# Kernel tuning notes

Measured on AMD Instinct MI355X. Metric: run time of the kernel, lower is better.

Reference implementation:

```python
import jax, jax.numpy as jnp
import numpy as np

B, C, F = 1024, 63, 250
H, D = 4, 250          # heads, out_channels per head
TOP_K = 8
NEG_SLOPE = 0.2


def setup_inputs() -> dict:
    key = jax.random.key(0)
    ks = jax.random.split(key, 7)
    x = jax.random.normal(ks[0], (B, 1, C, F), dtype=jnp.float32)
    W_gat = jax.random.normal(ks[1], (F, H * D), dtype=jnp.float32) / jnp.sqrt(jnp.float32(F))
    att_src = jax.random.normal(ks[2], (H, D), dtype=jnp.float32) * 0.1
    att_dst = jax.random.normal(ks[3], (H, D), dtype=jnp.float32) * 0.1
    bias_gat = jax.random.normal(ks[4], (H * D,), dtype=jnp.float32) * 0.02
    W_proj = jax.random.normal(ks[5], (H * D, D), dtype=jnp.float32) / jnp.sqrt(jnp.float32(H * D))
    b_proj = jax.random.normal(ks[6], (D,), dtype=jnp.float32) * 0.02
    return {"x": x, "W_gat": W_gat, "att_src": att_src, "att_dst": att_dst,
            "bias_gat": bias_gat, "W_proj": W_proj, "b_proj": b_proj}


def reference(x, W_gat, att_src, att_dst, bias_gat, W_proj, b_proj):
    # ---- correlation adjacency over the batch (non-differentiable mask path) ----
    xa = x[:, 0]                                             # [B, C, F]
    xc = xa - xa.mean(axis=-1, keepdims=True)
    xn = xc / (jnp.std(xc, axis=-1, ddof=1, keepdims=True) + 1e-8)  # unbiased std like torch
    adj = jnp.einsum('bcf,bdf->bcd', xn, xn) / jnp.float32(F)       # bmm / Fdim
    adj = adj.mean(axis=0)                                   # [C, C]
    topv, _ = jax.lax.top_k(adj, TOP_K)                      # per-row top-k
    thresh = topv[:, -1:]                                    # [C, 1]
    mask = (adj >= thresh) & (adj != 0)                      # nonzeros kept by dense_to_sparse
    eye = jnp.eye(C, dtype=bool)
    # GATConv: remove_self_loops then add_self_loops -> exactly one self loop per node
    mask_full = (mask & ~eye) | eye                          # [i(src), j(dst)]

    # ---- GATConv (edge_attr ignored: edge_dim=None -> lin_edge is None) ----
    h = (x.reshape(B * C, F) @ W_gat).reshape(B, C, H, D)    # [B, C, H, D]
    # edges only connect nodes 0..C-1 of the flattened (B*C) node tensor = batch 0
    h0 = h[0]                                                # [C, H, D]
    a_s = jnp.einsum('chd,hd->ch', h0, att_src)              # source logits
    a_d = jnp.einsum('chd,hd->ch', h0, att_dst)              # destination logits
    e = jax.nn.leaky_relu(a_s[:, None, :] + a_d[None, :, :], NEG_SLOPE)  # [i, j, h]
    logits = jnp.where(mask_full[:, :, None], e, -jnp.inf)
    w = jax.nn.softmax(logits, axis=0)                       # normalize over sources i per target j
    att0 = jnp.einsum('ijh,ihd->jhd', w, h0)                 # [C, H, D]
    # nodes >= C have only a self loop -> softmax weight 1 -> output = h
    y = h.at[0].set(att0)
    y = y.reshape(B * C, H * D) + bias_gat

    out = y @ W_proj + b_proj                                # [B*C, D]
    return out.reshape(B, C, -1)[:, None]                    # [B, 1, C, D]
```

## Files before the change

kernel.cpp:

```cpp
#include <hip/hip_runtime.h>
#include <math.h>

#define NB 1024
#define NC 63
#define NF 250
#define NH 4
#define ND 250
#define NHD 1000

typedef __bf16 bf16x8 __attribute__((ext_vector_type(8)));
typedef float f32x4 __attribute__((ext_vector_type(4)));

__global__ __launch_bounds__(256) void k_fused(const float* __restrict__ x,
                                               const __bf16* __restrict__ WcT,
                                               const float* __restrict__ biasc,
                                               float* __restrict__ out,
                                               float* __restrict__ partial) {
    __shared__ __align__(16) __bf16 Xh[64 * 256];
    __shared__ __align__(16) __bf16 Xl[64 * 256];
    float* const momS = (float*)Xh;
    const int t = threadIdx.x;
    const int w = t >> 6, l = t & 63;
    const int l16 = l & 15, lq = l >> 4;
    const int swz = (l16 & 7) << 3;
    const int nb = w * 64;

    {
        const int kz = t ^ 56;
        Xh[63 * 256 + kz] = (__bf16)1.0f;
        Xl[63 * 256 + kz] = (__bf16)0.0f;
    }

    float bc[4];
#pragma unroll
    for (int ni = 0; ni < 4; ++ni) {
        const int col = nb + ni * 16 + l16;
        bc[ni] = (col < ND) ? biasc[col] : 0.f;
    }

    const f32x4 z4 = {0.f, 0.f, 0.f, 0.f};
    const int b = blockIdx.x;
    const float* xb = x + (size_t)b * (NC * NF);

#pragma unroll
    for (int it = 0; it < 8; ++it) {
        const int u = it * 256 + t;
        if (u < 2016) {
            const int row = u >> 5;
            const int ko = (u & 31) << 3;
            const float* src = xb + row * NF + ko;
            float v[8];
#pragma unroll
            for (int q = 0; q < 4; ++q) {
                if (ko + q * 2 < NF) {
                    const float2 p = *(const float2*)(src + q * 2);
                    v[2 * q] = p.x; v[2 * q + 1] = p.y;
                } else { v[2 * q] = 0.f; v[2 * q + 1] = 0.f; }
            }
            bf16x8 h, lo_;
#pragma unroll
            for (int j = 0; j < 8; ++j) {
                h[j] = (__bf16)v[j];
                lo_[j] = (__bf16)(v[j] - (float)h[j]);
            }
            const int kS = ko ^ ((row & 7) << 3);
            *(bf16x8*)&Xh[row * 256 + kS] = h;
            *(bf16x8*)&Xl[row * 256 + kS] = lo_;
        }
    }
    __syncthreads();

    bf16x8 bfr[4][4];
    f32x4 accM[4][4];
    f32x4 accG[4];
#pragma unroll
    for (int mi = 0; mi < 4; ++mi)
#pragma unroll
        for (int ni = 0; ni < 4; ++ni) accM[mi][ni] = z4;
#pragma unroll
    for (int ni = 0; ni < 4; ++ni) accG[ni] = z4;

    const int garow = (16 * w + l16) * 256;

#pragma unroll
    for (int ni = 0; ni < 4; ++ni) {
        const int n = nb + ni * 16 + l16;
#pragma unroll
        for (int kk = 0; kk < 4; ++kk)
            bfr[ni][kk] = *(const bf16x8*)(WcT + (size_t)n * 256 + kk * 32 + lq * 8);
    }
#pragma unroll
    for (int kk = 0; kk < 4; ++kk) {
        const int kb = (kk * 32 + lq * 8) ^ swz;
        bf16x8 hi[4], lo[4];
#pragma unroll
        for (int r = 0; r < 4; ++r) {
            hi[r] = *(const bf16x8*)&Xh[(r * 16 + l16) * 256 + kb];
            lo[r] = *(const bf16x8*)&Xl[(r * 16 + l16) * 256 + kb];
        }
        const bf16x8 ah = *(const bf16x8*)&Xh[garow + kb];
        const bf16x8 al = *(const bf16x8*)&Xl[garow + kb];
#pragma unroll
        for (int mi = 0; mi < 4; ++mi)
#pragma unroll
            for (int ni = 0; ni < 4; ++ni)
                accM[mi][ni] = __builtin_amdgcn_mfma_f32_16x16x32_bf16(
                    hi[mi], bfr[ni][kk], accM[mi][ni], 0, 0, 0);
#pragma unroll
        for (int ni = 0; ni < 4; ++ni) {
            accG[ni] = __builtin_amdgcn_mfma_f32_16x16x32_bf16(ah, hi[ni], accG[ni], 0, 0, 0);
            accG[ni] = __builtin_amdgcn_mfma_f32_16x16x32_bf16(ah, lo[ni], accG[ni], 0, 0, 0);
            accG[ni] = __builtin_amdgcn_mfma_f32_16x16x32_bf16(al, hi[ni], accG[ni], 0, 0, 0);
        }
    }

#pragma unroll
    for (int ni = 0; ni < 4; ++ni) {
        const int n = nb + ni * 16 + l16;
#pragma unroll
        for (int kk = 0; kk < 4; ++kk)
            bfr[ni][kk] = *(const bf16x8*)(WcT + (size_t)n * 256 + (4 + kk) * 32 + lq * 8);
    }
#pragma unroll
    for (int kk = 0; kk < 4; ++kk) {
        const int kb = ((4 + kk) * 32 + lq * 8) ^ swz;
        bf16x8 hi[4], lo[4];
#pragma unroll
        for (int r = 0; r < 4; ++r) {
            hi[r] = *(const bf16x8*)&Xh[(r * 16 + l16) * 256 + kb];
            lo[r] = *(const bf16x8*)&Xl[(r * 16 + l16) * 256 + kb];
        }
        const bf16x8 ah = *(const bf16x8*)&Xh[garow + kb];
        const bf16x8 al = *(const bf16x8*)&Xl[garow + kb];
#pragma unroll
        for (int mi = 0; mi < 4; ++mi)
#pragma unroll
            for (int ni = 0; ni < 4; ++ni)
                accM[mi][ni] = __builtin_amdgcn_mfma_f32_16x16x32_bf16(
                    hi[mi], bfr[ni][kk], accM[mi][ni], 0, 0, 0);
#pragma unroll
        for (int ni = 0; ni < 4; ++ni) {
            accG[ni] = __builtin_amdgcn_mfma_f32_16x16x32_bf16(ah, hi[ni], accG[ni], 0, 0, 0);
            accG[ni] = __builtin_amdgcn_mfma_f32_16x16x32_bf16(ah, lo[ni], accG[ni], 0, 0, 0);
            accG[ni] = __builtin_amdgcn_mfma_f32_16x16x32_bf16(al, hi[ni], accG[ni], 0, 0, 0);
        }
    }

    __syncthreads();

    if (l16 == 15) {
#pragma unroll
        for (int r = 0; r < 4; ++r) momS[16 * w + lq * 4 + r] = accG[3][r];
    }
    if ((l16 >> 2) == lq) momS[64 + 16 * w + l16] = accG[w][l16 & 3];
    __syncthreads();
    if (t < 64) {
        const float S = momS[t], SSv = momS[64 + t];
        float m = S * (1.f / (float)NF);
        const float var = (SSv - S * S * (1.f / (float)NF)) * (1.f / (float)(NF - 1));
        float sc = 1.f / (sqrtf(var) + 1e-8f);
        if (t >= NC) { m = 0.f; sc = 0.f; }
        momS[128 + t] = m; momS[192 + t] = sc;
    }
    __syncthreads();

    float mr[4], sr[4];
#pragma unroll
    for (int r = 0; r < 4; ++r) {
        const int row = 16 * w + lq * 4 + r;
        mr[r] = momS[128 + row]; sr[r] = momS[192 + row];
    }
#pragma unroll
    for (int ni = 0; ni < 4; ++ni) {
        const float mc = momS[128 + 16 * ni + l16];
        const float sc = momS[192 + 16 * ni + l16];
#pragma unroll
        for (int r = 0; r < 4; ++r) {
            const int row = 16 * w + lq * 4 + r;
            const int col = 16 * ni + l16;
            partial[(size_t)b * 4096 + row * 64 + col] =
                (accG[ni][r] - (float)NF * mr[r] * mc) * sr[r] * sc;
        }
    }

    const size_t ob = (size_t)b * NC;
#pragma unroll
    for (int mi = 0; mi < 4; ++mi) {
#pragma unroll
        for (int r = 0; r < 4; ++r) {
            const int rt = mi * 16 + lq * 4 + r;
            if (rt < NC) {
#pragma unroll
                for (int ni = 0; ni < 4; ++ni) {
                    const int col = nb + ni * 16 + l16;
                    if (col < ND)
                        out[(ob + rt) * ND + col] = accM[mi][ni][r] + bc[ni];
                }
            }
        }
    }
}

__global__ __launch_bounds__(512) void k_adj_reduce(const float* __restrict__ partial,
                                                    float* __restrict__ adj) {
    __shared__ float red[8][64];
    const int row = blockIdx.x, t = threadIdx.x;
    const int c = t & 63, g = t >> 6;
    float s = 0.f;
    const float* p = partial + (size_t)(g * 128) * 4096 + row * 64 + c;
#pragma unroll 8
    for (int i = 0; i < 128; ++i) s += p[(size_t)i * 4096];
    red[g][c] = s;
    __syncthreads();
    if (t < NC) {
        float tot = 0.f;
#pragma unroll
        for (int gg = 0; gg < 8; ++gg) tot += red[gg][t];
        adj[row * NC + t] = tot * (1.f / ((float)NF * (float)NB));
    }
}

__global__ __launch_bounds__(256) void k_gs(const float* __restrict__ Wg,
                                            const float* __restrict__ att_src,
                                            const float* __restrict__ att_dst,
                                            float* __restrict__ gs,
                                            float* __restrict__ gd) {
    const int f = blockIdx.x;
    const int h = threadIdx.x >> 6, l = threadIdx.x & 63;
    const float* wr = Wg + (size_t)f * NHD + h * ND;
    const float* sp = att_src + h * ND;
    const float* dp = att_dst + h * ND;
    float s = 0.f, d = 0.f;
#pragma unroll
    for (int q = 0; q < 4; ++q) {
        const int dd = l + q * 64;
        if (dd < ND) {
            const float wv = wr[dd];
            s += wv * sp[dd];
            d += wv * dp[dd];
        }
    }
#pragma unroll
    for (int off = 32; off >= 1; off >>= 1) {
        s += __shfl_down(s, off);
        d += __shfl_down(d, off);
    }
    if (l == 0) { gs[f * NH + h] = s; gd[f * NH + h] = d; }
}

__global__ __launch_bounds__(512) void k_asad(const float* __restrict__ x,
                                              const float* __restrict__ gs,
                                              const float* __restrict__ gd,
                                              float* __restrict__ as_,
                                              float* __restrict__ ad_) {
    __shared__ float x0S[NC * NF];
    __shared__ float gsS[NF * NH], gdS[NF * NH];
    const int t = threadIdx.x;
    for (int e = t; e < NC * NF; e += 512) x0S[e] = x[e];
    for (int e = t; e < NF * NH; e += 512) { gsS[e] = gs[e]; gdS[e] = gd[e]; }
    __syncthreads();
    if (t < NC * NH) {
        const int c = t >> 2, h = t & 3;
        float s = 0.f, d = 0.f;
#pragma unroll 5
        for (int f = 0; f < NF; ++f) {
            const float xv = x0S[c * NF + f];
            s += xv * gsS[f * NH + h];
            d += xv * gdS[f * NH + h];
        }
        as_[t] = s; ad_[t] = d;
    }
}

__global__ __launch_bounds__(512) void k_out0(const float* __restrict__ adj,
                                              const float* __restrict__ as_,
                                              const float* __restrict__ ad_,
                                              const float* __restrict__ hp,
                                              const float* __restrict__ biasc,
                                              float* __restrict__ out) {
    __shared__ float adjS[NC * NC];
    __shared__ float thS[NC];
    __shared__ float asS[NC * 5];
    __shared__ float adS[NC * NH];
    __shared__ float wS[256];
    __shared__ float psum[2][256];
    const int j = blockIdx.x, t = threadIdx.x;
    const int w = t >> 6, l = t & 63;

    for (int e = t; e < NC * NC; e += 512) adjS[e] = adj[e];
    if (t < NC * NH) { asS[(t >> 2) * 5 + (t & 3)] = as_[t]; adS[t] = ad_[t]; }
    __syncthreads();

    for (int r = w; r < NC; r += 8) {
        const float v = (l < NC) ? adjS[r * NC + l] : -INFINITY;
        float prev = INFINITY;
        int krem = 8;
        float th = -INFINITY;
#pragma unroll
        for (int iter = 0; iter < 8; ++iter) {
            const float vm = (v < prev) ? v : -INFINITY;
            float m = vm;
#pragma unroll
            for (int off = 32; off >= 1; off >>= 1) m = fmaxf(m, __shfl_xor(m, off));
            const unsigned long long b = __ballot(vm == m);
            const int cnt = __popcll(b);
            if (cnt >= krem) { th = m; break; }
            krem -= cnt; prev = m;
        }
        if (l == 0) thS[r] = th;
    }
    __syncthreads();

    if (w < NH) {
        const int h = w, i = l;
        const float adv = adS[j * NH + h];
        const float a = (i < NC) ? adjS[i * NC + j] : 0.f;
        const bool msk = (i < NC) && ((i == j) || ((a >= thS[i]) && (a != 0.f)));
        float e = 0.f;
        if (msk) { e = asS[i * 5 + h] + adv; e = e > 0.f ? e : 0.2f * e; }
        float m = msk ? e : -INFINITY;
#pragma unroll
        for (int off = 32; off >= 1; off >>= 1) m = fmaxf(m, __shfl_xor(m, off));
        const float p = msk ? __expf(e - m) : 0.f;
        float s = p;
#pragma unroll
        for (int off = 32; off >= 1; off >>= 1) s += __shfl_xor(s, off);
        wS[(h << 6) + l] = p / s;
    }
    __syncthreads();

    const int q = t >> 8, col = t & 255;
    float acc = 0.f;
    const float* hpc = hp + col;
#pragma unroll 8
    for (int e = q * 128; e < q * 128 + 128; ++e)
        acc += wS[e] * hpc[(size_t)e * 256];
    psum[q][col] = acc;
    __syncthreads();
    if (t < ND) out[(size_t)j * ND + t] = psum[0][t] + psum[1][t] + biasc[t];
}

__global__ __launch_bounds__(256) void k_wc_part(const float* __restrict__ Wg,
                                                 const float* __restrict__ bias_gat,
                                                 const float* __restrict__ Wp,
                                                 float* __restrict__ pWcT,
                                                 float* __restrict__ pbias) {
    __shared__ float rows[250];
    const int b = blockIdx.x, t = threadIdx.x;
    if (b < 1000) {
        const int fb = (b >> 3) * 2, kq = b & 7;
        if (t < 250)
            rows[t] = Wg[(size_t)(fb + t / 125) * NHD + kq * 125 + (t % 125)];
        __syncthreads();
        if (t < ND) {
            float a0 = 0.f, a1 = 0.f;
            const float* wp = Wp + (size_t)(kq * 125) * ND + t;
            for (int k = 0; k < 125; ++k) {
                float wv = wp[(size_t)k * ND];
                a0 += rows[k] * wv;
                a1 += rows[125 + k] * wv;
            }
            pWcT[(size_t)kq * 65536 + (size_t)t * 256 + fb] = a0;
            pWcT[(size_t)kq * 65536 + (size_t)t * 256 + fb + 1] = a1;
        }
    } else {
        const int kq = b - 1000;
        if (t < ND) {
            float acc = 0.f;
            for (int k = kq * 125; k < kq * 125 + 125; ++k)
                acc += bias_gat[k] * Wp[(size_t)k * ND + t];
            pbias[kq * 256 + t] = acc;
        }
    }
}

__global__ __launch_bounds__(256) void k_wct(const float* __restrict__ pWcT,
                                             const float* __restrict__ pbias,
                                             const float* __restrict__ b_proj,
                                             __bf16* __restrict__ WcT,
                                             __bf16* __restrict__ WchT,
                                             float* __restrict__ biasc) {
    const int n = blockIdx.x, t = threadIdx.x;
    if (n < 256) {
        float v[8];
        float tot = 0.f;
#pragma unroll
        for (int kq = 0; kq < 8; ++kq) {
            float xv = 0.f;
            if (n < ND && t < NF) xv = pWcT[(size_t)kq * 65536 + (size_t)n * 256 + t];
            v[kq] = xv; tot += xv;
        }
        WcT[n * 256 + t] = (__bf16)tot;
#pragma unroll
        for (int h = 0; h < NH; ++h)
            WchT[h * 65536 + n * 256 + t] = (__bf16)(v[2 * h] + v[2 * h + 1]);
    } else {
        if (t < ND) {
            float v = 0.f;
#pragma unroll
            for (int kq = 0; kq < 8; ++kq) v += pbias[kq * 256 + t];
            biasc[t] = v + b_proj[t];
        }
    }
}

__global__ __launch_bounds__(256) void k_hp(const float* __restrict__ x,
                                            const __bf16* __restrict__ WchT,
                                            float* __restrict__ hp) {
    __shared__ __align__(16) __bf16 Xs[64 * 256];
    const int h = blockIdx.x;
    const int t = threadIdx.x;
    const int w = t >> 6, l = t & 63;
    const int l16 = l & 15, lq = l >> 4;
    const int nb = w * 64;
    const int swz = (l16 & 7) << 3;

    bf16x8 bfr[4][8];
    const __bf16* Wh = WchT + h * 65536;
#pragma unroll
    for (int ni = 0; ni < 4; ++ni) {
        const int n = nb + ni * 16 + l16;
#pragma unroll
        for (int kc = 0; kc < 8; ++kc)
            bfr[ni][kc] = *(const bf16x8*)(Wh + (size_t)n * 256 + kc * 32 + lq * 8);
    }

#pragma unroll
    for (int it = 0; it < 8; ++it) {
        const int u = it * 256 + t;
        const int row = u >> 5;
        const int ko = (u & 31) << 3;
        float v[8];
#pragma unroll
        for (int q = 0; q < 4; ++q) { v[2 * q] = 0.f; v[2 * q + 1] = 0.f; }
        if (row < NC) {
            const float* src = x + row * NF + ko;
#pragma unroll
            for (int q = 0; q < 4; ++q) {
                if (ko + 2 * q + 1 < NF) {
                    const float2 p = *(const float2*)(src + 2 * q);
                    v[2 * q] = p.x; v[2 * q + 1] = p.y;
                }
            }
        }
        bf16x8 hv;
#pragma unroll
        for (int jj = 0; jj < 8; ++jj) hv[jj] = (__bf16)v[jj];
        *(bf16x8*)&Xs[row * 256 + (ko ^ ((row & 7) << 3))] = hv;
    }
    __syncthreads();

    f32x4 acc[4][4];
    const f32x4 z4 = {0.f, 0.f, 0.f, 0.f};
#pragma unroll
    for (int mi = 0; mi < 4; ++mi)
#pragma unroll
        for (int ni = 0; ni < 4; ++ni) acc[mi][ni] = z4;

#pragma unroll
    for (int kc = 0; kc < 8; ++kc) {
        const int kb = (kc * 32 + lq * 8) ^ swz;
        bf16x8 afr[4];
#pragma unroll
        for (int mi = 0; mi < 4; ++mi)
            afr[mi] = *(const bf16x8*)&Xs[(mi * 16 + l16) * 256 + kb];
#pragma unroll
        for (int mi = 0; mi < 4; ++mi)
#pragma unroll
            for (int ni = 0; ni < 4; ++ni)
                acc[mi][ni] = __builtin_amdgcn_mfma_f32_16x16x32_bf16(
                    afr[mi], bfr[ni][kc], acc[mi][ni], 0, 0, 0);
    }

#pragma unroll
    for (int mi = 0; mi < 4; ++mi)
#pragma unroll
        for (int r = 0; r < 4; ++r) {
            const int row = mi * 16 + lq * 4 + r;
#pragma unroll
            for (int ni = 0; ni < 4; ++ni) {
                const int col = nb + ni * 16 + l16;
                hp[(size_t)(h * 64 + row) * 256 + col] = acc[mi][ni][r];
            }
        }
}

extern "C" void kernel_launch(void* const* d_in, const int* in_sizes, int n_in,
                              void* d_out, int out_size, void* d_ws, size_t ws_size,
                              hipStream_t stream) {
    const float* x       = (const float*)d_in[0];
    const float* Wg      = (const float*)d_in[1];
    const float* att_src = (const float*)d_in[2];
    const float* att_dst = (const float*)d_in[3];
    const float* bias_g  = (const float*)d_in[4];
    const float* Wp      = (const float*)d_in[5];
    const float* b_proj  = (const float*)d_in[6];
    float* out = (float*)d_out;
    float* ws  = (float*)d_ws;

    __bf16* WcT    = (__bf16*)ws;
    __bf16* WchT   = (__bf16*)(ws + 32768);
    float* pWcT    = ws + 32768 + 131072;
    float* pbias   = pWcT + 8 * 65536;
    float* biasc   = pbias + 2048;
    float* partial = biasc + 256;
    float* adj     = partial + 1024 * 4096;
    float* hp      = adj + NC * NC;
    float* gs      = hp + 65536;
    float* gd      = gs + 1000;
    float* as_     = gd + 1000;
    float* ad_     = as_ + 252;

    k_wc_part<<<1008, 256, 0, stream>>>(Wg, bias_g, Wp, pWcT, pbias);
    k_wct<<<257, 256, 0, stream>>>(pWcT, pbias, b_proj, WcT, WchT, biasc);
    k_fused<<<1024, 256, 0, stream>>>(x, WcT, biasc, out, partial);
    k_adj_reduce<<<63, 512, 0, stream>>>(partial, adj);
    k_gs<<<250, 256, 0, stream>>>(Wg, att_src, att_dst, gs, gd);
    k_asad<<<1, 512, 0, stream>>>(x, gs, gd, as_, ad_);
    k_hp<<<4, 256, 0, stream>>>(x, WchT, hp);
    k_out0<<<63, 512, 0, stream>>>(adj, as_, ad_, hp, biasc, out);
}
```

Before: 122.4 us.

## Stage X in two K-halves to halve shared memory and raise occupancy

Shared tiles for the hi/lo bf16 split of x shrink from 256 to 128 columns. The K dimension is now loaded and consumed in two halves, with a barrier between them. The ones-row used for moment sums is rebuilt per half and masked past F. Launch bounds now request 4 blocks per CU. The aim is to fit more concurrent blocks so global loads of one block overlap MFMA work of others. In exchange there is an extra sync and serialized load/compute phases within each block, and register pressure may force spills under the tighter bound.

```diff
diff --git a/kernel.cpp b/kernel.cpp
--- a/kernel.cpp
+++ b/kernel.cpp
@@ -11,13 +11,13 @@
 typedef __bf16 bf16x8 __attribute__((ext_vector_type(8)));
 typedef float f32x4 __attribute__((ext_vector_type(4)));
 
-__global__ __launch_bounds__(256) void k_fused(const float* __restrict__ x,
-                                               const __bf16* __restrict__ WcT,
-                                               const float* __restrict__ biasc,
-                                               float* __restrict__ out,
-                                               float* __restrict__ partial) {
-    __shared__ __align__(16) __bf16 Xh[64 * 256];
-    __shared__ __align__(16) __bf16 Xl[64 * 256];
+__global__ __launch_bounds__(256, 4) void k_fused(const float* __restrict__ x,
+                                                  const __bf16* __restrict__ WcT,
+                                                  const float* __restrict__ biasc,
+                                                  float* __restrict__ out,
+                                                  float* __restrict__ partial) {
+    __shared__ __align__(16) __bf16 Xh[64 * 128];
+    __shared__ __align__(16) __bf16 Xl[64 * 128];
     float* const momS = (float*)Xh;
     const int t = threadIdx.x;
     const int w = t >> 6, l = t & 63;
@@ -25,12 +25,6 @@
     const int swz = (l16 & 7) << 3;
     const int nb = w * 64;
 
-    {
-        const int kz = t ^ 56;
-        Xh[63 * 256 + kz] = (__bf16)1.0f;
-        Xl[63 * 256 + kz] = (__bf16)0.0f;
-    }
-
     float bc[4];
 #pragma unroll
     for (int ni = 0; ni < 4; ++ni) {
@@ -41,34 +35,7 @@
     const f32x4 z4 = {0.f, 0.f, 0.f, 0.f};
     const int b = blockIdx.x;
     const float* xb = x + (size_t)b * (NC * NF);
-
-#pragma unroll
-    for (int it = 0; it < 8; ++it) {
-        const int u = it * 256 + t;
-        if (u < 2016) {
-            const int row = u >> 5;
-            const int ko = (u & 31) << 3;
-            const float* src = xb + row * NF + ko;
-            float v[8];
-#pragma unroll
-            for (int q = 0; q < 4; ++q) {
-                if (ko + q * 2 < NF) {
-                    const float2 p = *(const float2*)(src + q * 2);
-                    v[2 * q] = p.x; v[2 * q + 1] = p.y;
-                } else { v[2 * q] = 0.f; v[2 * q + 1] = 0.f; }
-            }
-            bf16x8 h, lo_;
-#pragma unroll
-            for (int j = 0; j < 8; ++j) {
-                h[j] = (__bf16)v[j];
-                lo_[j] = (__bf16)(v[j] - (float)h[j]);
-            }
-            const int kS = ko ^ ((row & 7) << 3);
-            *(bf16x8*)&Xh[row * 256 + kS] = h;
-            *(bf16x8*)&Xl[row * 256 + kS] = lo_;
-        }
-    }
-    __syncthreads();
+    const int garow = (16 * w + l16) * 128;
 
     bf16x8 bfr[4][4];
     f32x4 accM[4][4];
@@ -80,69 +47,75 @@
 #pragma unroll
     for (int ni = 0; ni < 4; ++ni) accG[ni] = z4;
 
-    const int garow = (16 * w + l16) * 256;
-
-#pragma unroll
-    for (int ni = 0; ni < 4; ++ni) {
-        const int n = nb + ni * 16 + l16;
-#pragma unroll
-        for (int kk = 0; kk < 4; ++kk)
-            bfr[ni][kk] = *(const bf16x8*)(WcT + (size_t)n * 256 + kk * 32 + lq * 8);
-    }
-#pragma unroll
-    for (int kk = 0; kk < 4; ++kk) {
-        const int kb = (kk * 32 + lq * 8) ^ swz;
-        bf16x8 hi[4], lo[4];
-#pragma unroll
-        for (int r = 0; r < 4; ++r) {
-            hi[r] = *(const bf16x8*)&Xh[(r * 16 + l16) * 256 + kb];
-            lo[r] = *(const bf16x8*)&Xl[(r * 16 + l16) * 256 + kb];
-        }
-        const bf16x8 ah = *(const bf16x8*)&Xh[garow + kb];
-        const bf16x8 al = *(const bf16x8*)&Xl[garow + kb];
-#pragma unroll
-        for (int mi = 0; mi < 4; ++mi)
-#pragma unroll
-            for (int ni = 0; ni < 4; ++ni)
-                accM[mi][ni] = __builtin_amdgcn_mfma_f32_16x16x32_bf16(
-                    hi[mi], bfr[ni][kk], accM[mi][ni], 0, 0, 0);
+#pragma unroll
+    for (int h = 0; h < 2; ++h) {
+        if (h) __syncthreads();
+
+#pragma unroll
+        for (int it = 0; it < 4; ++it) {
+            const int u = it * 256 + t;
+            if (u < 1008) {
+                const int row = u >> 4;
+                const int ko = (u & 15) << 3;
+                const int kg = h * 128 + ko;
+                const float* src = xb + row * NF + kg;
+                float v[8];
+#pragma unroll
+                for (int q = 0; q < 4; ++q) {
+                    if (kg + q * 2 + 1 < NF) {
+                        const float2 p = *(const float2*)(src + q * 2);
+                        v[2 * q] = p.x; v[2 * q + 1] = p.y;
+                    } else { v[2 * q] = 0.f; v[2 * q + 1] = 0.f; }
+                }
+                bf16x8 hv, lo_;
+#pragma unroll
+                for (int j = 0; j < 8; ++j) {
+                    hv[j] = (__bf16)v[j];
+                    lo_[j] = (__bf16)(v[j] - (float)hv[j]);
+                }
+                const int kS = ko ^ ((row & 7) << 3);
+                *(bf16x8*)&Xh[row * 128 + kS] = hv;
+                *(bf16x8*)&Xl[row * 128 + kS] = lo_;
+            }
+        }
+        if (t < 128) {
+            const int kz = t ^ 56;
+            Xh[63 * 128 + kz] = (h * 128 + t < NF) ? (__bf16)1.0f : (__bf16)0.0f;
+            Xl[63 * 128 + kz] = (__bf16)0.0f;
+        }
+        __syncthreads();
+
 #pragma unroll
         for (int ni = 0; ni < 4; ++ni) {
-            accG[ni] = __builtin_amdgcn_mfma_f32_16x16x32_bf16(ah, hi[ni], accG[ni], 0, 0, 0);
-            accG[ni] = __builtin_amdgcn_mfma_f32_16x16x32_bf16(ah, lo[ni], accG[ni], 0, 0, 0);
-            accG[ni] = __builtin_amdgcn_mfma_f32_16x16x32_bf16(al, hi[ni], accG[ni], 0, 0, 0);
-        }
-    }
-
-#pragma unroll
-    for (int ni = 0; ni < 4; ++ni) {
-        const int n = nb + ni * 16 + l16;
-#pragma unroll
-        for (int kk = 0; kk < 4; ++kk)
-            bfr[ni][kk] = *(const bf16x8*)(WcT + (size_t)n * 256 + (4 + kk) * 32 + lq * 8);
-    }
-#pragma unroll
-    for (int kk = 0; kk < 4; ++kk) {
-        const int kb = ((4 + kk) * 32 + lq * 8) ^ swz;
-        bf16x8 hi[4], lo[4];
-#pragma unroll
-        for (int r = 0; r < 4; ++r) {
-            hi[r] = *(const bf16x8*)&Xh[(r * 16 + l16) * 256 + kb];
-            lo[r] = *(const bf16x8*)&Xl[(r * 16 + l16) * 256 + kb];
-        }
-        const bf16x8 ah = *(const bf16x8*)&Xh[garow + kb];
-        const bf16x8 al = *(const bf16x8*)&Xl[garow + kb];
-#pragma unroll
-        for (int mi = 0; mi < 4; ++mi)
-#pragma unroll
-            for (int ni = 0; ni < 4; ++ni)
-                accM[mi][ni] = __builtin_amdgcn_mfma_f32_16x16x32_bf16(
-                    hi[mi], bfr[ni][kk], accM[mi][ni], 0, 0, 0);
-#pragma unroll
-        for (int ni = 0; ni < 4; ++ni) {
-            accG[ni] = __builtin_amdgcn_mfma_f32_16x16x32_bf16(ah, hi[ni], accG[ni], 0, 0, 0);
-            accG[ni] = __builtin_amdgcn_mfma_f32_16x16x32_bf16(ah, lo[ni], accG[ni], 0, 0, 0);
-            accG[ni] = __builtin_amdgcn_mfma_f32_16x16x32_bf16(al, hi[ni], accG[ni], 0, 0, 0);
+            const int n = nb + ni * 16 + l16;
+#pragma unroll
+            for (int kk = 0; kk < 4; ++kk)
+                bfr[ni][kk] = *(const bf16x8*)(WcT + (size_t)n * 256 + (h * 4 + kk) * 32 + lq * 8);
+        }
+
+#pragma unroll
+        for (int kk = 0; kk < 4; ++kk) {
+            const int kb = (kk * 32 + lq * 8) ^ swz;
+            bf16x8 hi[4], lo[4];
+#pragma unroll
+            for (int r = 0; r < 4; ++r) {
+                hi[r] = *(const bf16x8*)&Xh[(r * 16 + l16) * 128 + kb];
+                lo[r] = *(const bf16x8*)&Xl[(r * 16 + l16) * 128 + kb];
+            }
+            const bf16x8 ah = *(const bf16x8*)&Xh[garow + kb];
+            const bf16x8 al = *(const bf16x8*)&Xl[garow + kb];
+#pragma unroll
+            for (int mi = 0; mi < 4; ++mi)
+#pragma unroll
+                for (int ni = 0; ni < 4; ++ni)
+                    accM[mi][ni] = __builtin_amdgcn_mfma_f32_16x16x32_bf16(
+                        hi[mi], bfr[ni][kk], accM[mi][ni], 0, 0, 0);
+#pragma unroll
+            for (int ni = 0; ni < 4; ++ni) {
+                accG[ni] = __builtin_amdgcn_mfma_f32_16x16x32_bf16(ah, hi[ni], accG[ni], 0, 0, 0);
+                accG[ni] = __builtin_amdgcn_mfma_f32_16x16x32_bf16(ah, lo[ni], accG[ni], 0, 0, 0);
+                accG[ni] = __builtin_amdgcn_mfma_f32_16x16x32_bf16(al, hi[ni], accG[ni], 0, 0, 0);
+            }
         }
     }
 
```

After: 159.0 us. +29.9%, slower.

## Merge small independent kernels into fewer launches via block-index dispatch

Applied to the files above, without the earlier changes.

Independent small kernels are merged into shared launches, with blockIdx ranges selecting the role: gs/gd computation joins the Wc partial product, the hp MFMA projection joins the Wc reduction (summing the fp32 partials directly instead of going through a bf16 WchT buffer), and adj reduction joins as/ad computation. This cuts the launch count from eight to five, removing launch gaps and serialization in a pipeline of mostly tiny kernels. The cost is heterogeneous blocks that may load-imbalance, and the combined adj/asad kernel now reserves large shared memory for every block.

```diff
diff --git a/kernel.cpp b/kernel.cpp
--- a/kernel.cpp
+++ b/kernel.cpp
@@ -201,74 +201,223 @@
     }
 }
 
-__global__ __launch_bounds__(512) void k_adj_reduce(const float* __restrict__ partial,
-                                                    float* __restrict__ adj) {
-    __shared__ float red[8][64];
-    const int row = blockIdx.x, t = threadIdx.x;
-    const int c = t & 63, g = t >> 6;
-    float s = 0.f;
-    const float* p = partial + (size_t)(g * 128) * 4096 + row * 64 + c;
+__global__ __launch_bounds__(256) void k_gswc(const float* __restrict__ Wg,
+                                              const float* __restrict__ att_src,
+                                              const float* __restrict__ att_dst,
+                                              const float* __restrict__ bias_gat,
+                                              const float* __restrict__ Wp,
+                                              float* __restrict__ pWcT,
+                                              float* __restrict__ pbias,
+                                              float* __restrict__ gs,
+                                              float* __restrict__ gd) {
+    __shared__ float rows[250];
+    const int b = blockIdx.x, t = threadIdx.x;
+    if (b < 1000) {
+        const int fb = (b >> 3) * 2, kq = b & 7;
+        if (t < 250)
+            rows[t] = Wg[(size_t)(fb + t / 125) * NHD + kq * 125 + (t % 125)];
+        __syncthreads();
+        if (t < ND) {
+            float a0 = 0.f, a1 = 0.f;
+            const float* wp = Wp + (size_t)(kq * 125) * ND + t;
+            for (int k = 0; k < 125; ++k) {
+                float wv = wp[(size_t)k * ND];
+                a0 += rows[k] * wv;
+                a1 += rows[125 + k] * wv;
+            }
+            pWcT[(size_t)kq * 65536 + (size_t)t * 256 + fb] = a0;
+            pWcT[(size_t)kq * 65536 + (size_t)t * 256 + fb + 1] = a1;
+        }
+    } else if (b < 1008) {
+        const int kq = b - 1000;
+        if (t < ND) {
+            float acc = 0.f;
+            for (int k = kq * 125; k < kq * 125 + 125; ++k)
+                acc += bias_gat[k] * Wp[(size_t)k * ND + t];
+            pbias[kq * 256 + t] = acc;
+        }
+    } else {
+        const int f = b - 1008;
+        const int h = t >> 6, l = t & 63;
+        const float* wr = Wg + (size_t)f * NHD + h * ND;
+        const float* sp = att_src + h * ND;
+        const float* dp = att_dst + h * ND;
+        float s = 0.f, d = 0.f;
+#pragma unroll
+        for (int q = 0; q < 4; ++q) {
+            const int dd = l + q * 64;
+            if (dd < ND) {
+                const float wv = wr[dd];
+                s += wv * sp[dd];
+                d += wv * dp[dd];
+            }
+        }
+#pragma unroll
+        for (int off = 32; off >= 1; off >>= 1) {
+            s += __shfl_down(s, off);
+            d += __shfl_down(d, off);
+        }
+        if (l == 0) { gs[f * NH + h] = s; gd[f * NH + h] = d; }
+    }
+}
+
+__global__ __launch_bounds__(256) void k_wcthp(const float* __restrict__ pWcT,
+                                               const float* __restrict__ pbias,
+                                               const float* __restrict__ b_proj,
+                                               const float* __restrict__ x,
+                                               __bf16* __restrict__ WcT,
+                                               float* __restrict__ biasc,
+                                               float* __restrict__ hp) {
+    __shared__ __align__(16) __bf16 Xs[64 * 256];
+    const int bidx = blockIdx.x, t = threadIdx.x;
+    if (bidx < 256) {
+        const int n = bidx;
+        float tot = 0.f;
+        if (n < ND && t < NF) {
+            size_t e = (size_t)n * 256 + t;
+#pragma unroll
+            for (int kq = 0; kq < 8; ++kq) tot += pWcT[(size_t)kq * 65536 + e];
+        }
+        WcT[n * 256 + t] = (__bf16)tot;
+    } else if (bidx == 256) {
+        if (t < ND) {
+            float v = 0.f;
+#pragma unroll
+            for (int kq = 0; kq < 8; ++kq) v += pbias[kq * 256 + t];
+            biasc[t] = v + b_proj[t];
+        }
+    } else {
+        const int h = bidx - 257;
+        const int w = t >> 6, l = t & 63;
+        const int l16 = l & 15, lq = l >> 4;
+        const int nb = w * 64;
+        const int swz = (l16 & 7) << 3;
+        const float* p0 = pWcT + (size_t)(2 * h) * 65536;
+        const float* p1 = pWcT + (size_t)(2 * h + 1) * 65536;
+
+        bf16x8 bfr[4][8];
+#pragma unroll
+        for (int ni = 0; ni < 4; ++ni) {
+            const int n = nb + ni * 16 + l16;
+#pragma unroll
+            for (int kc = 0; kc < 8; ++kc) {
+                const size_t base = (size_t)n * 256 + kc * 32 + lq * 8;
+                bf16x8 r;
+#pragma unroll
+                for (int j = 0; j < 8; ++j) {
+                    const int f = kc * 32 + lq * 8 + j;
+                    float v = 0.f;
+                    if (n < ND && f < NF) v = p0[base + j] + p1[base + j];
+                    r[j] = (__bf16)v;
+                }
+                bfr[ni][kc] = r;
+            }
+        }
+
+#pragma unroll
+        for (int it = 0; it < 8; ++it) {
+            const int u = it * 256 + t;
+            const int row = u >> 5;
+            const int ko = (u & 31) << 3;
+            float v[8];
+#pragma unroll
+            for (int q = 0; q < 4; ++q) { v[2 * q] = 0.f; v[2 * q + 1] = 0.f; }
+            if (row < NC) {
+                const float* src = x + row * NF + ko;
+#pragma unroll
+                for (int q = 0; q < 4; ++q) {
+                    if (ko + 2 * q + 1 < NF) {
+                        const float2 p = *(const float2*)(src + 2 * q);
+                        v[2 * q] = p.x; v[2 * q + 1] = p.y;
+                    }
+                }
+            }
+            bf16x8 hv;
+#pragma unroll
+            for (int jj = 0; jj < 8; ++jj) hv[jj] = (__bf16)v[jj];
+            *(bf16x8*)&Xs[row * 256 + (ko ^ ((row & 7) << 3))] = hv;
+        }
+        __syncthreads();
+
+        f32x4 acc[4][4];
+        const f32x4 z4 = {0.f, 0.f, 0.f, 0.f};
+#pragma unroll
+        for (int mi = 0; mi < 4; ++mi)
+#pragma unroll
+            for (int ni = 0; ni < 4; ++ni) acc[mi][ni] = z4;
+
+#pragma unroll
+        for (int kc = 0; kc < 8; ++kc) {
+            const int kb = (kc * 32 + lq * 8) ^ swz;
+            bf16x8 afr[4];
+#pragma unroll
+            for (int mi = 0; mi < 4; ++mi)
+                afr[mi] = *(const bf16x8*)&Xs[(mi * 16 + l16) * 256 + kb];
+#pragma unroll
+            for (int mi = 0; mi < 4; ++mi)
+#pragma unroll
+                for (int ni = 0; ni < 4; ++ni)
+                    acc[mi][ni] = __builtin_amdgcn_mfma_f32_16x16x32_bf16(
+                        afr[mi], bfr[ni][kc], acc[mi][ni], 0, 0, 0);
+        }
+
+#pragma unroll
+        for (int mi = 0; mi < 4; ++mi)
+#pragma unroll
+            for (int r = 0; r < 4; ++r) {
+                const int row = mi * 16 + lq * 4 + r;
+#pragma unroll
+                for (int ni = 0; ni < 4; ++ni) {
+                    const int col = nb + ni * 16 + l16;
+                    hp[(size_t)(h * 64 + row) * 256 + col] = acc[mi][ni][r];
+                }
+            }
+    }
+}
+
+__global__ __launch_bounds__(512) void k_adjred_asad(const float* __restrict__ partial,
+                                                     const float* __restrict__ x,
+                                                     const float* __restrict__ gs,
+                                                     const float* __restrict__ gd,
+                                                     float* __restrict__ adj,
+                                                     float* __restrict__ as_,
+                                                     float* __restrict__ ad_) {
+    __shared__ float smem[NC * NF + 2 * NHD];
+    const int t = threadIdx.x;
+    if (blockIdx.x < 63) {
+        float (*red)[64] = (float(*)[64])smem;
+        const int row = blockIdx.x;
+        const int c = t & 63, g = t >> 6;
+        float s = 0.f;
+        const float* p = partial + (size_t)(g * 128) * 4096 + row * 64 + c;
 #pragma unroll 8
-    for (int i = 0; i < 128; ++i) s += p[(size_t)i * 4096];
-    red[g][c] = s;
-    __syncthreads();
-    if (t < NC) {
-        float tot = 0.f;
-#pragma unroll
-        for (int gg = 0; gg < 8; ++gg) tot += red[gg][t];
-        adj[row * NC + t] = tot * (1.f / ((float)NF * (float)NB));
-    }
-}
-
-__global__ __launch_bounds__(256) void k_gs(const float* __restrict__ Wg,
-                                            const float* __restrict__ att_src,
-                                            const float* __restrict__ att_dst,
-                                            float* __restrict__ gs,
-                                            float* __restrict__ gd) {
-    const int f = blockIdx.x;
-    const int h = threadIdx.x >> 6, l = threadIdx.x & 63;
-    const float* wr = Wg + (size_t)f * NHD + h * ND;
-    const float* sp = att_src + h * ND;
-    const float* dp = att_dst + h * ND;
-    float s = 0.f, d = 0.f;
-#pragma unroll
-    for (int q = 0; q < 4; ++q) {
-        const int dd = l + q * 64;
-        if (dd < ND) {
-            const float wv = wr[dd];
-            s += wv * sp[dd];
-            d += wv * dp[dd];
-        }
-    }
-#pragma unroll
-    for (int off = 32; off >= 1; off >>= 1) {
-        s += __shfl_down(s, off);
-        d += __shfl_down(d, off);
-    }
-    if (l == 0) { gs[f * NH + h] = s; gd[f * NH + h] = d; }
-}
-
-__global__ __launch_bounds__(512) void k_asad(const float* __restrict__ x,
-                                              const float* __restrict__ gs,
-                                              const float* __restrict__ gd,
-                                              float* __restrict__ as_,
-                                              float* __restrict__ ad_) {
-    __shared__ float x0S[NC * NF];
-    __shared__ float gsS[NF * NH], gdS[NF * NH];
-    const int t = threadIdx.x;
-    for (int e = t; e < NC * NF; e += 512) x0S[e] = x[e];
-    for (int e = t; e < NF * NH; e += 512) { gsS[e] = gs[e]; gdS[e] = gd[e]; }
-    __syncthreads();
-    if (t < NC * NH) {
-        const int c = t >> 2, h = t & 3;
-        float s = 0.f, d = 0.f;
+        for (int i = 0; i < 128; ++i) s += p[(size_t)i * 4096];
+        red[g][c] = s;
+        __syncthreads();
+        if (t < NC) {
+            float tot = 0.f;
+#pragma unroll
+            for (int gg = 0; gg < 8; ++gg) tot += red[gg][t];
+            adj[row * NC + t] = tot * (1.f / ((float)NF * (float)NB));
+        }
+    } else {
+        float* x0S = smem;
+        float* gsS = smem + NC * NF;
+        float* gdS = gsS + NHD;
+        for (int e = t; e < NC * NF; e += 512) x0S[e] = x[e];
+        for (int e = t; e < NF * NH; e += 512) { gsS[e] = gs[e]; gdS[e] = gd[e]; }
+        __syncthreads();
+        if (t < NC * NH) {
+            const int c = t >> 2, h = t & 3;
+            float s = 0.f, d = 0.f;
 #pragma unroll 5
-        for (int f = 0; f < NF; ++f) {
-            const float xv = x0S[c * NF + f];
-            s += xv * gsS[f * NH + h];
-            d += xv * gdS[f * NH + h];
-        }
-        as_[t] = s; ad_[t] = d;
+            for (int f = 0; f < NF; ++f) {
+                const float xv = x0S[c * NF + f];
+                s += xv * gsS[f * NH + h];
+                d += xv * gdS[f * NH + h];
+            }
+            as_[t] = s; ad_[t] = d;
+        }
     }
 }
 
@@ -302,8 +451,8 @@
             float m = vm;
 #pragma unroll
             for (int off = 32; off >= 1; off >>= 1) m = fmaxf(m, __shfl_xor(m, off));
-            const unsigned long long b = __ballot(vm == m);
-            const int cnt = __popcll(b);
+            const unsigned long long bl = __ballot(vm == m);
+            const int cnt = __popcll(bl);
             if (cnt >= krem) { th = m; break; }
             krem -= cnt; prev = m;
         }
@@ -338,151 +487,6 @@
     psum[q][col] = acc;
     __syncthreads();
     if (t < ND) out[(size_t)j * ND + t] = psum[0][t] + psum[1][t] + biasc[t];
-}
-
-__global__ __launch_bounds__(256) void k_wc_part(const float* __restrict__ Wg,
-                                                 const float* __restrict__ bias_gat,
-                                                 const float* __restrict__ Wp,
-                                                 float* __restrict__ pWcT,
-                                                 float* __restrict__ pbias) {
-    __shared__ float rows[250];
-    const int b = blockIdx.x, t = threadIdx.x;
-    if (b < 1000) {
-        const int fb = (b >> 3) * 2, kq = b & 7;
-        if (t < 250)
-            rows[t] = Wg[(size_t)(fb + t / 125) * NHD + kq * 125 + (t % 125)];
-        __syncthreads();
-        if (t < ND) {
-            float a0 = 0.f, a1 = 0.f;
-            const float* wp = Wp + (size_t)(kq * 125) * ND + t;
-            for (int k = 0; k < 125; ++k) {
-                float wv = wp[(size_t)k * ND];
-                a0 += rows[k] * wv;
-                a1 += rows[125 + k] * wv;
-            }
-            pWcT[(size_t)kq * 65536 + (size_t)t * 256 + fb] = a0;
-            pWcT[(size_t)kq * 65536 + (size_t)t * 256 + fb + 1] = a1;
-        }
-    } else {
-        const int kq = b - 1000;
-        if (t < ND) {
-            float acc = 0.f;
-            for (int k = kq * 125; k < kq * 125 + 125; ++k)
-                acc += bias_gat[k] * Wp[(size_t)k * ND + t];
-            pbias[kq * 256 + t] = acc;
-        }
-    }
-}
-
-__global__ __launch_bounds__(256) void k_wct(const float* __restrict__ pWcT,
-                                             const float* __restrict__ pbias,
-                                             const float* __restrict__ b_proj,
-                                             __bf16* __restrict__ WcT,
-                                             __bf16* __restrict__ WchT,
-                                             float* __restrict__ biasc) {
-    const int n = blockIdx.x, t = threadIdx.x;
-    if (n < 256) {
-        float v[8];
-        float tot = 0.f;
-#pragma unroll
-        for (int kq = 0; kq < 8; ++kq) {
-            float xv = 0.f;
-            if (n < ND && t < NF) xv = pWcT[(size_t)kq * 65536 + (size_t)n * 256 + t];
-            v[kq] = xv; tot += xv;
-        }
-        WcT[n * 256 + t] = (__bf16)tot;
-#pragma unroll
-        for (int h = 0; h < NH; ++h)
-            WchT[h * 65536 + n * 256 + t] = (__bf16)(v[2 * h] + v[2 * h + 1]);
-    } else {
-        if (t < ND) {
-            float v = 0.f;
-#pragma unroll
-            for (int kq = 0; kq < 8; ++kq) v += pbias[kq * 256 + t];
-            biasc[t] = v + b_proj[t];
-        }
-    }
-}
-
-__global__ __launch_bounds__(256) void k_hp(const float* __restrict__ x,
-                                            const __bf16* __restrict__ WchT,
-                                            float* __restrict__ hp) {
-    __shared__ __align__(16) __bf16 Xs[64 * 256];
-    const int h = blockIdx.x;
-    const int t = threadIdx.x;
-    const int w = t >> 6, l = t & 63;
-    const int l16 = l & 15, lq = l >> 4;
-    const int nb = w * 64;
-    const int swz = (l16 & 7) << 3;
-
-    bf16x8 bfr[4][8];
-    const __bf16* Wh = WchT + h * 65536;
-#pragma unroll
-    for (int ni = 0; ni < 4; ++ni) {
-        const int n = nb + ni * 16 + l16;
-#pragma unroll
-        for (int kc = 0; kc < 8; ++kc)
-            bfr[ni][kc] = *(const bf16x8*)(Wh + (size_t)n * 256 + kc * 32 + lq * 8);
-    }
-
-#pragma unroll
-    for (int it = 0; it < 8; ++it) {
-        const int u = it * 256 + t;
-        const int row = u >> 5;
-        const int ko = (u & 31) << 3;
-        float v[8];
-#pragma unroll
-        for (int q = 0; q < 4; ++q) { v[2 * q] = 0.f; v[2 * q + 1] = 0.f; }
-        if (row < NC) {
-            const float* src = x + row * NF + ko;
-#pragma unroll
-            for (int q = 0; q < 4; ++q) {
-                if (ko + 2 * q + 1 < NF) {
-                    const float2 p = *(const float2*)(src + 2 * q);
-                    v[2 * q] = p.x; v[2 * q + 1] = p.y;
-                }
-            }
-        }
-        bf16x8 hv;
-#pragma unroll
-        for (int jj = 0; jj < 8; ++jj) hv[jj] = (__bf16)v[jj];
-        *(bf16x8*)&Xs[row * 256 + (ko ^ ((row & 7) << 3))] = hv;
-    }
-    __syncthreads();
-
-    f32x4 acc[4][4];
-    const f32x4 z4 = {0.f, 0.f, 0.f, 0.f};
-#pragma unroll
-    for (int mi = 0; mi < 4; ++mi)
-#pragma unroll
-        for (int ni = 0; ni < 4; ++ni) acc[mi][ni] = z4;
-
-#pragma unroll
-    for (int kc = 0; kc < 8; ++kc) {
-        const int kb = (kc * 32 + lq * 8) ^ swz;
-        bf16x8 afr[4];
-#pragma unroll
-        for (int mi = 0; mi < 4; ++mi)
-            afr[mi] = *(const bf16x8*)&Xs[(mi * 16 + l16) * 256 + kb];
-#pragma unroll
-        for (int mi = 0; mi < 4; ++mi)
-#pragma unroll
-            for (int ni = 0; ni < 4; ++ni)
-                acc[mi][ni] = __builtin_amdgcn_mfma_f32_16x16x32_bf16(
-                    afr[mi], bfr[ni][kc], acc[mi][ni], 0, 0, 0);
-    }
-
-#pragma unroll
-    for (int mi = 0; mi < 4; ++mi)
-#pragma unroll
-        for (int r = 0; r < 4; ++r) {
-            const int row = mi * 16 + lq * 4 + r;
-#pragma unroll
-            for (int ni = 0; ni < 4; ++ni) {
-                const int col = nb + ni * 16 + l16;
-                hp[(size_t)(h * 64 + row) * 256 + col] = acc[mi][ni][r];
-            }
-        }
 }
 
 extern "C" void kernel_launch(void* const* d_in, const int* in_sizes, int n_in,
@@ -499,8 +503,7 @@
     float* ws  = (float*)d_ws;
 
     __bf16* WcT    = (__bf16*)ws;
-    __bf16* WchT   = (__bf16*)(ws + 32768);
-    float* pWcT    = ws + 32768 + 131072;
+    float* pWcT    = ws + 32768;
     float* pbias   = pWcT + 8 * 65536;
     float* biasc   = pbias + 2048;
     float* partial = biasc + 256;
@@ -511,12 +514,10 @@
     float* as_     = gd + 1000;
     float* ad_     = as_ + 252;
 
-    k_wc_part<<<1008, 256, 0, stream>>>(Wg, bias_g, Wp, pWcT, pbias);
-    k_wct<<<257, 256, 0, stream>>>(pWcT, pbias, b_proj, WcT, WchT, biasc);
+    k_gswc<<<1258, 256, 0, stream>>>(Wg, att_src, att_dst, bias_g, Wp,
+                                     pWcT, pbias, gs, gd);
+    k_wcthp<<<261, 256, 0, stream>>>(pWcT, pbias, b_proj, x, WcT, biasc, hp);
     k_fused<<<1024, 256, 0, stream>>>(x, WcT, biasc, out, partial);
-    k_adj_reduce<<<63, 512, 0, stream>>>(partial, adj);
-    k_gs<<<250, 256, 0, stream>>>(Wg, att_src, att_dst, gs, gd);
-    k_asad<<<1, 512, 0, stream>>>(x, gs, gd, as_, ad_);
-    k_hp<<<4, 256, 0, stream>>>(x, WchT, hp);
+    k_adjred_asad<<<64, 512, 0, stream>>>(partial, x, gs, gd, adj, as_, ad_);
     k_out0<<<63, 512, 0, stream>>>(adj, as_, ad_, hp, biasc, out);
 }
```

New measurement: 163.4 us. 1.34x slower.
